# Performance work log

Measured on AMD Instinct MI355X. Metric: run time of the kernel, lower is better.

## Reference

```python
import jax, jax.numpy as jnp
import numpy as np

B, Tc, E, K, M, V = 8, 1024, 256, 8, 2048, 16
T1 = Tc * K          # penultimate layer length = 8192
TLAST = M * K        # last layer length = 16384


def setup_inputs() -> dict:
    key = jax.random.key(0)
    ks = jax.random.split(key, 12)
    x = jax.random.normal(ks[0], (B, Tc, E), jnp.float32)
    # penultimate values: exactly M 'mixed' tokens (value==2) per row, rest in {1,3}
    base = jnp.where(jnp.arange(T1) < M, 2, 1 + 2 * jax.random.randint(ks[1], (B, T1), 0, 2))
    perm = jnp.argsort(jax.random.uniform(ks[2], (B, T1)), axis=1)
    val1 = jnp.take_along_axis(base, perm, axis=1)
    vallast = 1 + 2 * jax.random.randint(ks[3], (B, TLAST), 0, 2)
    value = jnp.concatenate([val1, vallast], axis=1).astype(jnp.int64)
    depth = jnp.concatenate([jnp.full((B, T1), 5), jnp.full((B, TLAST), 6)], axis=1).astype(jnp.int64)
    pos = jax.random.randint(ks[4], (B, T1 + TLAST, 3), 0, 64).astype(jnp.int64)
    s = 0.02
    W1 = s * jax.random.normal(ks[5], (E, E, K), jnp.float32)  # ConvTranspose1d weight [in,out,k]
    b1 = s * jax.random.normal(ks[6], (E,), jnp.float32)
    W0 = s * jax.random.normal(ks[7], (E, E, K), jnp.float32)
    b0 = s * jax.random.normal(ks[8], (E,), jnp.float32)
    Wl = s * jax.random.normal(ks[9], (V + 1, E), jnp.float32)
    bl = s * jax.random.normal(ks[10], (V + 1,), jnp.float32)
    return {"x": x, "value": value, "depth": depth, "pos": pos, "num_mix": M,
            "W1": W1, "b1": b1, "W0": W0, "b0": b0, "Wl": Wl, "bl": bl}


def _deconv(x, W, b):
    # ConvTranspose1d with kernel=stride=K: each token expands to K tokens
    n, t, e = x.shape
    o = W.shape[1]
    y = jnp.einsum('nte,eoj->ntjo', x, W)  # [N,T,K,O]
    return y.reshape(n, t * W.shape[2], o) + b


def reference(x, value, depth, pos, num_mix, W1, b1, W0, b0, Wl, bl):
    n, tc, e = x.shape
    k = W1.shape[2]
    t1 = tc * k
    max_depth = jnp.max(depth)
    len_1 = jnp.sum(depth == max_depth - 1, axis=1)               # [N]
    tt = jnp.arange(t1)
    val_1 = jnp.where(tt[None, :] < len_1[:, None], value[:, :t1], 0)  # padded penultimate values
    mix_mask = val_1 == 2                                         # [N,T1]
    mix_1 = jnp.sum(mix_mask, axis=1)                             # [N]
    y_1 = _deconv(x, W1, b1)                                      # [N,T1,E]
    # stable pack: bring positions with value==2 to the front, keep order
    order = jnp.argsort(jnp.where(mix_mask, 0, 1), axis=1, stable=True)
    sel = order[:, :num_mix]                                      # [N,M]
    x_0 = jnp.take_along_axis(y_1, sel[:, :, None], axis=1)       # [N,M,E]
    valid = (jnp.arange(num_mix)[None, :] < mix_1[:, None]).astype(x_0.dtype)
    x_0 = x_0 * valid[:, :, None]                                 # zero-pad beyond per-row mix count
    y_0 = _deconv(x_0, W0, b0)                                    # [N,M*K,E]
    return y_0 @ Wl.T + bl                                        # [N,M*K,V+1]
```

## Files before the change

kernel.cpp:

```cpp
#include <hip/hip_runtime.h>

typedef __attribute__((ext_vector_type(8))) short bf16x8;
typedef __attribute__((ext_vector_type(4))) float f32x4;

#define BB 8
#define TC 1024
#define EE 256
#define KJ 8
#define MSEL 2048
#define V1 17
#define T1 8192
#define TTOT 24576
#define BI_TOT 16384
#define NCOLP 160
#define WSTRIDE 264
#define GSZ 40960

__device__ __forceinline__ int pk_idx(int col, int e) {
    return (((col >> 4) * 8 + (e >> 5)) << 9) + (((e >> 3) & 3) << 7) + ((col & 15) << 3) + (e & 7);
}

#define SCAL_OFF 0
#define GRP_OFF  1024
#define WFT_OFF  (GRP_OFF + 524288)
#define B2_OFF   (WFT_OFF + GSZ*2)
#define BF0_OFF  (B2_OFF + 640)
#define WCT_OFF  (BF0_OFF + 128)

__device__ __forceinline__ unsigned short f2bf(float f) {
    union { float f; unsigned u; } x; x.f = f;
    unsigned r = x.u + 0x7fffu + ((x.u >> 16) & 1u);
    return (unsigned short)(r >> 16);
}
__device__ __forceinline__ float bf2f(unsigned short h) {
    union { unsigned u; float f; } x; x.u = ((unsigned)h) << 16;
    return x.f;
}

__device__ __forceinline__ float blockReduceSum256(float v) {
    __shared__ float sm[4];
    #pragma unroll
    for (int d = 32; d; d >>= 1) v += __shfl_down(v, d, 64);
    int lane = threadIdx.x & 63, wid = threadIdx.x >> 6;
    if (lane == 0) sm[wid] = v;
    __syncthreads();
    float r = sm[0] + sm[1] + sm[2] + sm[3];
    __syncthreads();
    return r;
}

__global__ __launch_bounds__(256) void k_pre(const float* W0, const float* Wl, const int* depth,
                                             unsigned short* wfT, int* scal) {
    int bid = blockIdx.x, tid = threadIdx.x;
    __shared__ float w0s[EE * KJ];
    __shared__ float wls[V1 * 257];
    __shared__ int s_red[4];
    if (bid < 256) {
        int em = bid;
        for (int idx = tid; idx < EE * KJ; idx += 256) w0s[idx] = W0[em * EE * KJ + idx];
        for (int idx = tid; idx < V1 * EE; idx += 256) {
            int v = idx >> 8, o = idx & 255;
            wls[v * 257 + o] = Wl[idx];
        }
        __syncthreads();
        if (tid < 136) {
            int j = tid / V1, v = tid - j * V1;
            float acc = 0.f;
            #pragma unroll 4
            for (int o = 0; o < EE; ++o) acc += w0s[o * KJ + j] * wls[v * 257 + o];
            wfT[pk_idx(j * 20 + v, em)] = f2bf(acc);
        }
    } else {
        int b = bid - 256;
        if (b == 0 && tid < 8) scal[33 + tid] = 0;
        const int4* dp = (const int4*)(depth + b * TTOT);
        int m = -2147483648;
        for (int i = tid; i < 6144; i += 256) {
            int4 d = dp[i];
            m = max(max(m, max(d.x, d.y)), max(d.z, d.w));
        }
        #pragma unroll
        for (int dd = 32; dd; dd >>= 1) m = max(m, __shfl_down(m, dd, 64));
        if ((tid & 63) == 0) s_red[tid >> 6] = m;
        __syncthreads();
        int bmax = max(max(s_red[0], s_red[1]), max(s_red[2], s_red[3]));
        if (tid == 0) scal[1 + b] = bmax;
        int c1 = 0, c2 = 0;
        for (int i = tid; i < 6144; i += 256) {
            int4 d = dp[i];
            c1 += (d.x == bmax) + (d.y == bmax) + (d.z == bmax) + (d.w == bmax);
            c2 += (d.x == bmax - 1) + (d.y == bmax - 1) + (d.z == bmax - 1) + (d.w == bmax - 1);
        }
        int cc = (c1 << 16) + c2;
        #pragma unroll
        for (int dd = 32; dd; dd >>= 1) cc += __shfl_down(cc, dd, 64);
        __syncthreads();
        if ((tid & 63) == 0) s_red[tid >> 6] = cc;
        __syncthreads();
        if (tid == 0) {
            int tot = s_red[0] + s_red[1] + s_red[2] + s_red[3];
            scal[9 + b] = tot >> 16;
            scal[17 + b] = tot & 0xffff;
        }
    }
}

__global__ __launch_bounds__(256) void k_mid(
        const int* value, const float* W1, const float* b1, const float* b0,
        const float* Wl, const float* bl,
        int* scal, int* groups, const unsigned short* wfT, float* bias2, float* bf0,
        unsigned short* wct) {
    int bid = blockIdx.x, tid = threadIdx.x;
    __shared__ __align__(16) unsigned short b1s[32 * WSTRIDE];
    __shared__ int s_wt[4], s_lcnt[8], s_lcnt2[8], s_lbase[8];
    if (bid < 64) {
        int g = bid >> 3;
        int e0 = (bid & 7) * 32;
        {
            int em_l = tid & 63;
            int eb = (tid >> 6) * 8;
            #pragma unroll
            for (int i = 0; i < 8; ++i) {
                int e = eb + i;
                #pragma unroll
                for (int c = 0; c < 4; ++c) {
                    int em = c * 64 + em_l;
                    b1s[e * WSTRIDE + em] = f2bf(W1[(e0 + e) * (EE * KJ) + em * KJ + g]);
                }
            }
        }
        __syncthreads();

        int w = tid >> 6, l = tid & 63;
        int ntile = w & 1, mhalf = w >> 1;
        int lr = l & 15, lq = l >> 4;
        f32x4 acc[5];
        #pragma unroll
        for (int t = 0; t < 5; ++t) acc[t] = (f32x4){0.f, 0.f, 0.f, 0.f};

        #pragma unroll
        for (int ch = 0; ch < 4; ++ch) {
            #pragma unroll
            for (int s = 0; s < 2; ++s) {
                bf16x8 bfr = *(const bf16x8*)&b1s[(ntile * 16 + lr) * WSTRIDE + ch * 64 + s * 32 + lq * 8];
                #pragma unroll
                for (int t = 0; t < 5; ++t) {
                    bf16x8 afr = *(const bf16x8*)&wfT[(((mhalf * 5 + t) * 8 + ch * 2 + s) << 9) + l * 8];
                    acc[t] = __builtin_amdgcn_mfma_f32_16x16x32_bf16(afr, bfr, acc[t], 0, 0, 0);
                }
            }
        }
        #pragma unroll
        for (int t = 0; t < 5; ++t) {
            int ct = mhalf * 5 + t;
            int e = e0 + ntile * 16 + lr;
            #pragma unroll
            for (int r = 0; r < 4; ++r) {
                int col = ct * 16 + lq * 4 + r;
                wct[g * GSZ + pk_idx(col, e)] = f2bf(acc[t][r]);
            }
        }
    } else if (bid < 72) {
        int b = bid - 64;
        int mb = scal[1 + b], cm = scal[9 + b], cm1 = scal[17 + b];
        int gmax = scal[1];
        #pragma unroll
        for (int q = 2; q <= 8; ++q) gmax = max(gmax, scal[q]);
        int len1 = (mb == gmax) ? cm1 : ((mb == gmax - 1) ? cm : 0);
        const int* vb = value + b * TTOT;
        int t0 = tid * 32;
        unsigned mask = 0;
        #pragma unroll
        for (int k = 0; k < 32; k += 4) {
            int4 v = *(const int4*)(vb + t0 + k);
            if (t0 + k + 0 < len1 && v.x == 2) mask |= 1u << (k + 0);
            if (t0 + k + 1 < len1 && v.y == 2) mask |= 1u << (k + 1);
            if (t0 + k + 2 < len1 && v.z == 2) mask |= 1u << (k + 2);
            if (t0 + k + 3 < len1 && v.w == 2) mask |= 1u << (k + 3);
        }
        int cnt = __popc(mask);
        int inc = cnt;
        #pragma unroll
        for (int d = 1; d < 64; d <<= 1) {
            int n = __shfl_up(inc, d, 64);
            if ((tid & 63) >= d) inc += n;
        }
        int lane = tid & 63, wid = tid >> 6;
        if (lane == 63) s_wt[wid] = inc;
        if (tid < 8) { s_lcnt[tid] = 0; s_lcnt2[tid] = 0; }
        __syncthreads();
        int woff = 0;
        for (int w = 0; w < wid; ++w) woff += s_wt[w];
        int off0 = woff + inc - cnt;
        int mix1 = s_wt[0] + s_wt[1] + s_wt[2] + s_wt[3];
        int mix1c = min(mix1, MSEL);
        {
            int off = off0;
            #pragma unroll
            for (int k = 0; k < 32; ++k) {
                if (mask & (1u << k)) {
                    if (off < MSEL) atomicAdd(&s_lcnt[(t0 + k) & 7], 1);
                    off++;
                }
            }
        }
        if (tid == 0 && mix1c < MSEL) atomicAdd(&s_lcnt[0], MSEL - mix1c);
        __syncthreads();
        if (tid < 8) s_lbase[tid] = atomicAdd(&scal[33 + tid], s_lcnt[tid]);
        __syncthreads();
        {
            int off = off0;
            #pragma unroll
            for (int k = 0; k < 32; ++k) {
                if (mask & (1u << k)) {
                    if (off < MSEL) {
                        int t = t0 + k;
                        int g = t & 7;
                        int ls = atomicAdd(&s_lcnt2[g], 1);
                        groups[g * BI_TOT + s_lbase[g] + ls] =
                            ((b * MSEL + off) << 11) | ((t >> 3) << 1) | 1;
                    }
                    off++;
                }
            }
        }
        for (int i = mix1c + tid; i < MSEL; i += 256) {
            int ls = atomicAdd(&s_lcnt2[0], 1);
            groups[s_lbase[0] + ls] = (b * MSEL + i) << 11;
        }
    } else if (bid < 89) {
        int v = bid - 72;
        float s = blockReduceSum256(b0[tid] * Wl[v * EE + tid]);
        if (tid == 0) bf0[v] = s + bl[v];
    } else {
        #pragma unroll
        for (int r = 0; r < 2; ++r) {
            int c17 = (bid - 89) * 2 + r;
            int j = c17 / V1, v = c17 - j * V1;
            int colP = j * 20 + v;
            float s = blockReduceSum256(b1[tid] * bf2f(wfT[pk_idx(colP, tid)]));
            if (tid == 0) bias2[colP] = s;
        }
    }
}

__global__ __launch_bounds__(256) void k_main(const float* x, const unsigned short* wct,
        const int* scal, const int* groups, const float* bias2, const float* bf0, float* out) {
    int g = blockIdx.x >> 7;
    int tile0 = blockIdx.x & 127;
    int cntg = scal[33 + g];

    __shared__ __align__(16) unsigned short xs[32 * WSTRIDE];
    __shared__ int obase[32];
    __shared__ unsigned char vflag[32];
    int tid = threadIdx.x;
    int row8 = tid >> 3, q8 = tid & 7;
    int w = tid >> 6, l = tid & 63;
    int rw = w & 1, chalf = w >> 1;
    int lr = l & 15, lq = l >> 4;
    const unsigned short* wg = wct + g * GSZ;

    for (int tile = tile0; tile * 32 < cntg; tile += 128) {
        int nrows = min(32, cntg - tile * 32);
        __syncthreads();
        int pk = (row8 < nrows) ? groups[g * BI_TOT + tile * 32 + row8] : 0;
        if (tid < 32) {
            int p2 = (tid < nrows) ? groups[g * BI_TOT + tile * 32 + tid] : 0;
            obase[tid] = (p2 >> 11) * 136;
            vflag[tid] = (tid < nrows) ? (unsigned char)(1 + (p2 & 1)) : (unsigned char)0;
        }
        int bi = pk >> 11;
        int xo = ((bi >> 11) * TC + ((pk >> 1) & 1023)) * EE;
        const float* xp = x + xo;
        float4 xr[8];
        #pragma unroll
        for (int i = 0; i < 8; ++i) xr[i] = *(const float4*)(xp + (q8 + 8 * i) * 4);
        #pragma unroll
        for (int i = 0; i < 8; ++i) {
            ushort4 pkv;
            pkv.x = f2bf(xr[i].x); pkv.y = f2bf(xr[i].y);
            pkv.z = f2bf(xr[i].z); pkv.w = f2bf(xr[i].w);
            *(ushort4*)&xs[row8 * WSTRIDE + (q8 + 8 * i) * 4] = pkv;
        }
        __syncthreads();

        f32x4 acc[5];
        #pragma unroll
        for (int t = 0; t < 5; ++t) acc[t] = (f32x4){0.f, 0.f, 0.f, 0.f};
        #pragma unroll
        for (int ch = 0; ch < 4; ++ch) {
            #pragma unroll
            for (int s = 0; s < 2; ++s) {
                bf16x8 afr = *(const bf16x8*)&xs[(rw * 16 + lr) * WSTRIDE + ch * 64 + s * 32 + lq * 8];
                #pragma unroll
                for (int t = 0; t < 5; ++t) {
                    bf16x8 bfr = *(const bf16x8*)&wg[(((chalf * 5 + t) * 8 + ch * 2 + s) << 9) + l * 8];
                    acc[t] = __builtin_amdgcn_mfma_f32_16x16x32_bf16(afr, bfr, acc[t], 0, 0, 0);
                }
            }
        }
        #pragma unroll
        for (int t = 0; t < 5; ++t) {
            int col = (chalf * 5 + t) * 16 + lr;
            int j = col / 20, v = col % 20;
            if (v < V1) {
                float bb = bias2[col] + bf0[v];
                float b0v = bf0[v];
                #pragma unroll
                for (int r = 0; r < 4; ++r) {
                    int row = rw * 16 + lq * 4 + r;
                    int fl = vflag[row];
                    if (fl) out[obase[row] + j * V1 + v] = (fl == 2) ? (acc[t][r] + bb) : b0v;
                }
            }
        }
    }
}

extern "C" void kernel_launch(void* const* d_in, const int* in_sizes, int n_in,
                              void* d_out, int out_size, void* d_ws, size_t ws_size,
                              hipStream_t stream) {
    const float* x     = (const float*)d_in[0];
    const int*   value = (const int*)d_in[1];
    const int*   depth = (const int*)d_in[2];
    const float* W1    = (const float*)d_in[5];
    const float* b1    = (const float*)d_in[6];
    const float* W0    = (const float*)d_in[7];
    const float* b0    = (const float*)d_in[8];
    const float* Wl    = (const float*)d_in[9];
    const float* bl    = (const float*)d_in[10];
    float* out = (float*)d_out;
    char* ws = (char*)d_ws;

    int*            scal   = (int*)(ws + SCAL_OFF);
    int*            groups = (int*)(ws + GRP_OFF);
    unsigned short* wfT    = (unsigned short*)(ws + WFT_OFF);
    float*          bias2  = (float*)(ws + B2_OFF);
    float*          bf0    = (float*)(ws + BF0_OFF);
    unsigned short* wct    = (unsigned short*)(ws + WCT_OFF);

    k_pre <<<dim3(264),  dim3(256), 0, stream>>>(W0, Wl, depth, wfT, scal);
    k_mid <<<dim3(157),  dim3(256), 0, stream>>>(value, W1, b1, b0, Wl, bl,
                                                 scal, groups, wfT, bias2, bf0, wct);
    k_main<<<dim3(1024), dim3(256), 0, stream>>>(x, wct, scal, groups, bias2, bf0, out);
}
```

Before: 116.5 us.

## Merge three kernels into one cooperative kernel with grid-wide syncs

Folds the preprocessing, middle (weight fusion, grouping, biases) and main GEMM kernels into a single cooperative kernel of 512 blocks, with grid.sync() between phases. Shared memory is unioned across phases. The aim is to remove two kernel launch boundaries and their launch latency. In exchange the main phase now runs on 512 persistent blocks instead of 1024, so each handles twice as many tiles. Cooperative launch also requires all blocks to be co-resident, and the grid barriers have their own cost.

After: 231.7 us. +98.9%, slower.

```diff
diff --git a/kernel.cpp b/kernel.cpp
--- a/kernel.cpp
+++ b/kernel.cpp
@@ -1,4 +1,7 @@
 #include <hip/hip_runtime.h>
+#include <hip/hip_cooperative_groups.h>
+
+namespace cg = cooperative_groups;
 
 typedef __attribute__((ext_vector_type(8))) short bf16x8;
 typedef __attribute__((ext_vector_type(4))) float f32x4;
@@ -20,7 +23,6 @@
     return (((col >> 4) * 8 + (e >> 5)) << 9) + (((e >> 3) & 3) << 7) + ((col & 15) << 3) + (e & 7);
 }
 
-#define SCAL_OFF 0
 #define GRP_OFF  1024
 #define WFT_OFF  (GRP_OFF + 524288)
 #define B2_OFF   (WFT_OFF + GSZ*2)
@@ -38,39 +40,51 @@
 }
 
 __device__ __forceinline__ float blockReduceSum256(float v) {
-    __shared__ float sm[4];
+    __shared__ float smr[4];
     #pragma unroll
     for (int d = 32; d; d >>= 1) v += __shfl_down(v, d, 64);
     int lane = threadIdx.x & 63, wid = threadIdx.x >> 6;
-    if (lane == 0) sm[wid] = v;
+    if (lane == 0) smr[wid] = v;
     __syncthreads();
-    float r = sm[0] + sm[1] + sm[2] + sm[3];
+    float r = smr[0] + smr[1] + smr[2] + smr[3];
     __syncthreads();
     return r;
 }
 
-__global__ __launch_bounds__(256) void k_pre(const float* W0, const float* Wl, const int* depth,
-                                             unsigned short* wfT, int* scal) {
+__global__ __launch_bounds__(256, 2) void k_all(
+        const float* x, const int* value, const int* depth,
+        const float* W0, const float* W1, const float* b1, const float* b0,
+        const float* Wl, const float* bl,
+        int* scal, int* groups, unsigned short* wfT, float* bias2, float* bf0,
+        unsigned short* wct, float* out) {
     int bid = blockIdx.x, tid = threadIdx.x;
-    __shared__ float w0s[EE * KJ];
-    __shared__ float wls[V1 * 257];
+    __shared__ __align__(16) union SMem {
+        struct { float w0s[EE * KJ]; float wls[V1 * 257]; } p1;
+        unsigned short b1s[32 * WSTRIDE];
+        unsigned short xs[32 * WSTRIDE];
+    } smu;
     __shared__ int s_red[4];
+    __shared__ int s_wt[4], s_lcnt[8], s_lcnt2[8], s_lbase[8];
+    __shared__ int obase[32];
+    __shared__ unsigned char vflag[32];
+    cg::grid_group gg = cg::this_grid();
+
     if (bid < 256) {
         int em = bid;
-        for (int idx = tid; idx < EE * KJ; idx += 256) w0s[idx] = W0[em * EE * KJ + idx];
+        for (int idx = tid; idx < EE * KJ; idx += 256) smu.p1.w0s[idx] = W0[em * EE * KJ + idx];
         for (int idx = tid; idx < V1 * EE; idx += 256) {
             int v = idx >> 8, o = idx & 255;
-            wls[v * 257 + o] = Wl[idx];
+            smu.p1.wls[v * 257 + o] = Wl[idx];
         }
         __syncthreads();
         if (tid < 136) {
             int j = tid / V1, v = tid - j * V1;
             float acc = 0.f;
             #pragma unroll 4
-            for (int o = 0; o < EE; ++o) acc += w0s[o * KJ + j] * wls[v * 257 + o];
+            for (int o = 0; o < EE; ++o) acc += smu.p1.w0s[o * KJ + j] * smu.p1.wls[v * 257 + o];
             wfT[pk_idx(j * 20 + v, em)] = f2bf(acc);
         }
-    } else {
+    } else if (bid < 264) {
         int b = bid - 256;
         if (b == 0 && tid < 8) scal[33 + tid] = 0;
         const int4* dp = (const int4*)(depth + b * TTOT);
@@ -103,16 +117,8 @@
             scal[17 + b] = tot & 0xffff;
         }
     }
-}
-
-__global__ __launch_bounds__(256) void k_mid(
-        const int* value, const float* W1, const float* b1, const float* b0,
-        const float* Wl, const float* bl,
-        int* scal, int* groups, const unsigned short* wfT, float* bias2, float* bf0,
-        unsigned short* wct) {
-    int bid = blockIdx.x, tid = threadIdx.x;
-    __shared__ __align__(16) unsigned short b1s[32 * WSTRIDE];
-    __shared__ int s_wt[4], s_lcnt[8], s_lcnt2[8], s_lbase[8];
+    gg.sync();
+
     if (bid < 64) {
         int g = bid >> 3;
         int e0 = (bid & 7) * 32;
@@ -125,7 +131,7 @@
                 #pragma unroll
                 for (int c = 0; c < 4; ++c) {
                     int em = c * 64 + em_l;
-                    b1s[e * WSTRIDE + em] = f2bf(W1[(e0 + e) * (EE * KJ) + em * KJ + g]);
+                    smu.b1s[e * WSTRIDE + em] = f2bf(W1[(e0 + e) * (EE * KJ) + em * KJ + g]);
                 }
             }
         }
@@ -142,7 +148,7 @@
         for (int ch = 0; ch < 4; ++ch) {
             #pragma unroll
             for (int s = 0; s < 2; ++s) {
-                bf16x8 bfr = *(const bf16x8*)&b1s[(ntile * 16 + lr) * WSTRIDE + ch * 64 + s * 32 + lq * 8];
+                bf16x8 bfr = *(const bf16x8*)&smu.b1s[(ntile * 16 + lr) * WSTRIDE + ch * 64 + s * 32 + lq * 8];
                 #pragma unroll
                 for (int t = 0; t < 5; ++t) {
                     bf16x8 afr = *(const bf16x8*)&wfT[(((mhalf * 5 + t) * 8 + ch * 2 + s) << 9) + l * 8];
@@ -228,39 +234,32 @@
             int ls = atomicAdd(&s_lcnt2[0], 1);
             groups[s_lbase[0] + ls] = (b * MSEL + i) << 11;
         }
-    } else if (bid < 89) {
-        int v = bid - 72;
-        float s = blockReduceSum256(b0[tid] * Wl[v * EE + tid]);
-        if (tid == 0) bf0[v] = s + bl[v];
-    } else {
+    } else if (bid < 140) {
         #pragma unroll
         for (int r = 0; r < 2; ++r) {
-            int c17 = (bid - 89) * 2 + r;
+            int c17 = (bid - 72) * 2 + r;
             int j = c17 / V1, v = c17 - j * V1;
             int colP = j * 20 + v;
             float s = blockReduceSum256(b1[tid] * bf2f(wfT[pk_idx(colP, tid)]));
             if (tid == 0) bias2[colP] = s;
         }
+    } else if (bid < 157) {
+        int v = bid - 140;
+        float s = blockReduceSum256(b0[tid] * Wl[v * EE + tid]);
+        if (tid == 0) bf0[v] = s + bl[v];
     }
-}
-
-__global__ __launch_bounds__(256) void k_main(const float* x, const unsigned short* wct,
-        const int* scal, const int* groups, const float* bias2, const float* bf0, float* out) {
-    int g = blockIdx.x >> 7;
-    int tile0 = blockIdx.x & 127;
+    gg.sync();
+
+    int g = bid >> 6;
+    int slot = bid & 63;
     int cntg = scal[33 + g];
-
-    __shared__ __align__(16) unsigned short xs[32 * WSTRIDE];
-    __shared__ int obase[32];
-    __shared__ unsigned char vflag[32];
-    int tid = threadIdx.x;
     int row8 = tid >> 3, q8 = tid & 7;
     int w = tid >> 6, l = tid & 63;
     int rw = w & 1, chalf = w >> 1;
     int lr = l & 15, lq = l >> 4;
     const unsigned short* wg = wct + g * GSZ;
 
-    for (int tile = tile0; tile * 32 < cntg; tile += 128) {
+    for (int tile = slot; tile * 32 < cntg; tile += 64) {
         int nrows = min(32, cntg - tile * 32);
         __syncthreads();
         int pk = (row8 < nrows) ? groups[g * BI_TOT + tile * 32 + row8] : 0;
@@ -280,7 +279,7 @@
             ushort4 pkv;
             pkv.x = f2bf(xr[i].x); pkv.y = f2bf(xr[i].y);
             pkv.z = f2bf(xr[i].z); pkv.w = f2bf(xr[i].w);
-            *(ushort4*)&xs[row8 * WSTRIDE + (q8 + 8 * i) * 4] = pkv;
+            *(ushort4*)&smu.xs[row8 * WSTRIDE + (q8 + 8 * i) * 4] = pkv;
         }
         __syncthreads();
 
@@ -291,7 +290,7 @@
         for (int ch = 0; ch < 4; ++ch) {
             #pragma unroll
             for (int s = 0; s < 2; ++s) {
-                bf16x8 afr = *(const bf16x8*)&xs[(rw * 16 + lr) * WSTRIDE + ch * 64 + s * 32 + lq * 8];
+                bf16x8 afr = *(const bf16x8*)&smu.xs[(rw * 16 + lr) * WSTRIDE + ch * 64 + s * 32 + lq * 8];
                 #pragma unroll
                 for (int t = 0; t < 5; ++t) {
                     bf16x8 bfr = *(const bf16x8*)&wg[(((chalf * 5 + t) * 8 + ch * 2 + s) << 9) + l * 8];
@@ -332,15 +331,20 @@
     float* out = (float*)d_out;
     char* ws = (char*)d_ws;
 
-    int*            scal   = (int*)(ws + SCAL_OFF);
+    int*            scal   = (int*)(ws);
     int*            groups = (int*)(ws + GRP_OFF);
     unsigned short* wfT    = (unsigned short*)(ws + WFT_OFF);
     float*          bias2  = (float*)(ws + B2_OFF);
     float*          bf0    = (float*)(ws + BF0_OFF);
     unsigned short* wct    = (unsigned short*)(ws + WCT_OFF);
 
-    k_pre <<<dim3(264),  dim3(256), 0, stream>>>(W0, Wl, depth, wfT, scal);
-    k_mid <<<dim3(157),  dim3(256), 0, stream>>>(value, W1, b1, b0, Wl, bl,
-                                                 scal, groups, wfT, bias2, bf0, wct);
-    k_main<<<dim3(1024), dim3(256), 0, stream>>>(x, wct, scal, groups, bias2, bf0, out);
-}
+    void* args[] = {
+        (void*)&x, (void*)&value, (void*)&depth,
+        (void*)&W0, (void*)&W1, (void*)&b1, (void*)&b0,
+        (void*)&Wl, (void*)&bl,
+        (void*)&scal, (void*)&groups, (void*)&wfT, (void*)&bias2, (void*)&bf0,
+        (void*)&wct, (void*)&out
+    };
+    hipLaunchCooperativeKernel((const void*)k_all, dim3(512), dim3(256),
+                               args, 0, stream);
+}
```
